# Performance work log

Hardware: AMD Instinct MI355X
Metric: run time of the kernel (lower is better)

The kernel has to match this reference:

```python
import jax, jax.numpy as jnp
import numpy as np

K = 4096          # input_size
N = 12288         # output_size
M = 4096          # tokens (batch*seq)
GROUP_SIZE = 128  # EXL2 quantization group size along K
G = K // GROUP_SIZE


def setup_inputs() -> dict:
    key = jax.random.key(0)
    k1, k2, k3, k4, k5 = jax.random.split(key, 5)
    input_ = jax.random.normal(k1, (M, K), dtype=jnp.float16)
    # packed 4-bit weights: 8 nibbles per int32 along K -> [K//8, N]
    q_weight = jax.random.randint(k2, (K // 8, N), 0, 2147483647, dtype=jnp.int32)
    # packed 4-bit scale codes: 8 per int32 along N -> [G, N//8]
    q_scale = jax.random.randint(k3, (G, N // 8), 0, 2147483647, dtype=jnp.int32)
    # per-group max scale (post_init divides by 256)
    q_scale_max = (jax.random.uniform(k4, (G,), dtype=jnp.float32) / 256.0).astype(jnp.float16)
    q_invperm = jax.random.permutation(k5, jnp.arange(K, dtype=jnp.int32))
    bias = jnp.zeros((N,), dtype=jnp.float16)
    return {"input_": input_, "q_weight": q_weight, "q_scale": q_scale,
            "q_scale_max": q_scale_max, "q_invperm": q_invperm, "bias": bias}


def _dequant(q_weight, q_scale, q_scale_max):
    # unpack 8 4-bit weight codes per int32 along K
    shifts = jnp.arange(8, dtype=jnp.int32) * 4
    wn = (q_weight[:, None, :] >> shifts[None, :, None]) & 0xF   # [K//8, 8, N]
    wn = wn.reshape(K, N).astype(jnp.float32)
    # unpack 8 4-bit scale codes per int32 along N
    sn = (q_scale[:, :, None] >> shifts[None, None, :]) & 0xF    # [G, N//8, 8]
    sn = sn.reshape(G, N).astype(jnp.float32)
    # exllamav2 scale law: s = (code + 1)^2 * scale_max (per group)
    scale = (sn + 1.0) ** 2 * q_scale_max.astype(jnp.float32)[:, None]  # [G, N]
    scale = jnp.repeat(scale, GROUP_SIZE, axis=0)                # [K, N]
    return (wn - 8.0) * scale                                    # dequantized fp32 [K, N]


def reference(input_, q_weight, q_scale, q_scale_max, q_invperm, bias):
    W = _dequant(q_weight, q_scale, q_scale_max)                 # [K, N] fp32
    perm = jnp.argsort(q_invperm)                                # q_perm from post_init
    x = input_.astype(jnp.float32)[:, perm]                      # permuted activations [M, K]
    out = jnp.matmul(x, W).astype(jnp.float16)                   # fused dequant-GEMM result
    return out + bias
```

## Files before the change

### kernel.cpp

```cpp
#include <hip/hip_runtime.h>

#define Mdim 4096
#define Kdim 4096
#define Ndim 12288

typedef __bf16 bf16x8 __attribute__((ext_vector_type(8)));
typedef float f32x4 __attribute__((ext_vector_type(4)));
typedef unsigned short u16x8 __attribute__((ext_vector_type(8)));
typedef int i32x4 __attribute__((ext_vector_type(4)));

__device__ __forceinline__ unsigned short f2bf(float f) {
    unsigned int u = __builtin_bit_cast(unsigned int, f);
    u += 0x7FFFu + ((u >> 16) & 1u);
    return (unsigned short)(u >> 16);
}

typedef __attribute__((address_space(1))) void gvoid_t;
typedef __attribute__((address_space(3))) void lvoid_t;
__device__ __forceinline__ void gld16(const void* g, void* l) {
    __builtin_amdgcn_global_load_lds((gvoid_t*)g, (lvoid_t*)l, 16, 0, 0);
}

__global__ __launch_bounds__(256) void permute_convert_a_kernel(
    const float* __restrict__ A, const int* __restrict__ invperm,
    unsigned short* __restrict__ Ab)
{
    __shared__ unsigned short rowbuf[2][Kdim];
    const int tid = threadIdx.x;
    const int m0 = blockIdx.x * 2;
#pragma unroll
    for (int c = 0; c < 4; ++c) {
        const int i = (c * 256 + tid) * 4;
        const i32x4 ip = *(const i32x4*)&invperm[i];
        const f32x4 v0 = *(const f32x4*)&A[(size_t)m0 * Kdim + i];
        const f32x4 v1 = *(const f32x4*)&A[(size_t)(m0 + 1) * Kdim + i];
#pragma unroll
        for (int u = 0; u < 4; ++u) {
            rowbuf[0][ip[u]] = f2bf(v0[u]);
            rowbuf[1][ip[u]] = f2bf(v1[u]);
        }
    }
    __syncthreads();
#pragma unroll
    for (int r = 0; r < 2; ++r)
#pragma unroll
        for (int c = 0; c < 2; ++c) {
            const int j = (c * 256 + tid) * 8;
            const u16x8 o = *(const u16x8*)&rowbuf[r][j];
            *(u16x8*)&Ab[(size_t)(m0 + r) * Kdim + j] = o;
        }
}

__global__ __launch_bounds__(256) void dequant_kernel(
    const int* __restrict__ qw,
    const int* __restrict__ qs,
    const float* __restrict__ qsm,
    unsigned short* __restrict__ Wt)
{
    __shared__ unsigned short tile[64 * 72];
    const int k0 = blockIdx.x * 64;
    const int n0 = blockIdx.y * 64;
    const int g = k0 >> 7;
    const int tid = threadIdx.x;
    const int n_l = tid & 63;
    const int kb_l = tid >> 6;
    const int n = n0 + n_l;
    const int sw = qs[g * (Ndim / 8) + (n >> 3)];
    const int sc = (sw >> ((n & 7) * 4)) & 0xF;
    const float scale = (float)((sc + 1) * (sc + 1)) * qsm[g];
#pragma unroll
    for (int ii = 0; ii < 2; ++ii) {
        const int kb = kb_l + ii * 4;
        const int w = qw[(size_t)(k0 / 8 + kb) * Ndim + n];
        u16x8 o;
#pragma unroll
        for (int u = 0; u < 8; ++u)
            o[u] = f2bf((float)(((w >> (4 * u)) & 0xF) - 8) * scale);
        *(u16x8*)&tile[n_l * 72 + kb * 8] = o;
    }
    __syncthreads();
#pragma unroll
    for (int cc = 0; cc < 2; ++cc) {
        const int c = tid + cc * 256;
        const int row = c >> 3, part = c & 7;
        const u16x8 v = *(const u16x8*)&tile[row * 72 + part * 8];
        *(u16x8*)&Wt[(size_t)(n0 + row) * Kdim + k0 + part * 8] = v;
    }
}

#define BAR()    asm volatile("s_barrier" ::: "memory")
#define VMCNT8() asm volatile("s_waitcnt vmcnt(8)" ::: "memory")

#define STAGE(dstW, src, slot, koff) do {                                   \
    gld16((src) + (koff), (dstW) + (slot) * 8192);                          \
    gld16((src) + (koff) + rstep, (dstW) + (slot) * 8192 + 4096); } while (0)

#define LD_A(slot, mh) do {                                                 \
    const unsigned short* p_ = &As[slot][wm * 4096 + (mh) * 2048 + aOff];   \
    af[0] = *(const bf16x8*)(p_);                                           \
    af[1] = *(const bf16x8*)(p_ + 512);                                     \
    af[2] = *(const bf16x8*)(p_ + 1024);                                    \
    af[3] = *(const bf16x8*)(p_ + 1536); } while (0)

#define LD_B(slot) do {                                                     \
    const unsigned short* p_ = &Bs[slot][wn * 2048 + aOff];                 \
    bf[0] = *(const bf16x8*)(p_);                                           \
    bf[1] = *(const bf16x8*)(p_ + 512);                                     \
    bf[2] = *(const bf16x8*)(p_ + 1024);                                    \
    bf[3] = *(const bf16x8*)(p_ + 1536); } while (0)

#define MFMA_HALF(mh) do {                                                  \
    __builtin_amdgcn_s_setprio(1);                                          \
    _Pragma("unroll")                                                       \
    for (int i_ = 0; i_ < 4; ++i_)                                          \
      _Pragma("unroll")                                                     \
      for (int j_ = 0; j_ < 4; ++j_)                                        \
        acc[(mh) * 4 + i_][j_] = __builtin_amdgcn_mfma_f32_16x16x32_bf16(   \
            af[i_], bf[j_], acc[(mh) * 4 + i_][j_], 0, 0, 0);               \
    __builtin_amdgcn_s_setprio(0); } while (0)

__global__ __launch_bounds__(512, 2) void gemm_bf16_256_kernel(
    const unsigned short* __restrict__ A,
    const unsigned short* __restrict__ Bt,
    const float* __restrict__ bias,
    float* __restrict__ C)
{
    __shared__ __attribute__((aligned(16))) unsigned short As[4][8192];
    __shared__ __attribute__((aligned(16))) unsigned short Bs[4][8192];

    const int tid = threadIdx.x;
    const int lane = tid & 63, wave = tid >> 6;
    const int wm = wave >> 2, wn = wave & 3;

    const int wgid = (blockIdx.x & 7) * 96 + (blockIdx.x >> 3);
    const int bm = wgid & 15;
    const int bn = wgid >> 4;

    const int srow = 16 * wave + (lane & 15);
    const int skoff = (lane >> 4) * 8;
    const unsigned short* Ag = A + (size_t)(bm * 256 + srow) * Kdim + skoff;
    const unsigned short* Bg = Bt + (size_t)(bn * 256 + srow) * Kdim + skoff;
    const size_t rstep = (size_t)128 * Kdim;
    unsigned short* AsW = &As[0][0] + wave * 512;
    unsigned short* BsW = &Bs[0][0] + wave * 512;

    const int aOff = lane * 8;

    f32x4 acc[8][4];
    const f32x4 zero = {0.f, 0.f, 0.f, 0.f};
#pragma unroll
    for (int i = 0; i < 8; ++i)
#pragma unroll
        for (int j = 0; j < 4; ++j) acc[i][j] = zero;

    STAGE(AsW, Ag, 0, 0);
    STAGE(BsW, Bg, 0, 0);
    STAGE(AsW, Ag, 1, 32);
    STAGE(BsW, Bg, 1, 32);
    STAGE(AsW, Ag, 2, 64);
    STAGE(BsW, Bg, 2, 64);
    VMCNT8();
    BAR();

    bf16x8 af[4], bf[4];
#pragma unroll 2
    for (int t = 0; t < 64; ++t) {
        const int s0 = (2 * t) & 3, s1 = (2 * t + 1) & 3, sd1 = (2 * t + 3) & 3;
        const int tn1 = (t + 1 < 64 ? t + 1 : 63) * 64;
        const int tn2 = (t + 2 < 64 ? t + 2 : 63) * 64;
        LD_A(s0, 0);
        LD_B(s0);
        STAGE(AsW, Ag, sd1, tn1 + 32);
        BAR();
        MFMA_HALF(0);
        BAR();
        LD_A(s0, 1);
        STAGE(BsW, Bg, sd1, tn1 + 32);
        VMCNT8();
        BAR();
        MFMA_HALF(1);
        BAR();
        LD_A(s1, 0);
        LD_B(s1);
        STAGE(AsW, Ag, s0, tn2);
        BAR();
        MFMA_HALF(0);
        BAR();
        LD_A(s1, 1);
        STAGE(BsW, Bg, s0, tn2);
        VMCNT8();
        BAR();
        MFMA_HALF(1);
        BAR();
    }

    const int colb = bn * 256 + wn * 64 + (lane & 15);
    const int rowb = bm * 256 + wm * 128 + (lane >> 4) * 4;
    float bj[4];
#pragma unroll
    for (int j = 0; j < 4; ++j) bj[j] = bias[colb + j * 16];
#pragma unroll
    for (int mf = 0; mf < 8; ++mf)
#pragma unroll
        for (int r = 0; r < 4; ++r) {
            const size_t row = (size_t)(rowb + mf * 16 + r);
#pragma unroll
            for (int j = 0; j < 4; ++j)
                C[row * Ndim + colb + j * 16] = acc[mf][j][r] + bj[j];
        }
}

extern "C" void kernel_launch(void* const* d_in, const int* in_sizes, int n_in,
                              void* d_out, int out_size, void* d_ws, size_t ws_size,
                              hipStream_t stream) {
    const float* input   = (const float*)d_in[0];
    const int*   qw      = (const int*)d_in[1];
    const int*   qs      = (const int*)d_in[2];
    const float* qsm     = (const float*)d_in[3];
    const int*   invperm = (const int*)d_in[4];
    const float* bias    = (const float*)d_in[5];
    float*       out     = (float*)d_out;

    unsigned short* Ab = (unsigned short*)d_ws;
    unsigned short* Wt = (unsigned short*)((char*)d_ws + ((size_t)Mdim * Kdim * 2));

    permute_convert_a_kernel<<<Mdim / 2, 256, 0, stream>>>(input, invperm, Ab);
    dequant_kernel<<<dim3(Kdim / 64, Ndim / 64), 256, 0, stream>>>(qw, qs, qsm, Wt);
    gemm_bf16_256_kernel<<<dim3((Mdim / 256) * (Ndim / 256)), 512, 0, stream>>>(
        Ab, Wt, bias, out);
}
```

Before: 702.6 us.

## Pre-tile A and W into GEMM staging layout for contiguous LDS loads

The permute/convert and dequant kernels now write their bf16 outputs in a blocked layout that matches the GEMM's per-k-step LDS tile order. Each 32-wide k-slice of a 256-row block becomes one contiguous 16 KB chunk, so every thread's global_load_lds reads consecutive addresses instead of strided rows. The permute kernel now handles 16 rows per block to produce whole tiles. This is meant to cut address-translation and strided-fetch overhead in the GEMM main loop, at the cost of more scattered writes in the producer kernels and a larger LDS footprint in the permute kernel.

```diff
diff --git a/kernel.cpp b/kernel.cpp
--- a/kernel.cpp
+++ b/kernel.cpp
@@ -21,34 +21,34 @@
     __builtin_amdgcn_global_load_lds((gvoid_t*)g, (lvoid_t*)l, 16, 0, 0);
 }
 
-__global__ __launch_bounds__(256) void permute_convert_a_kernel(
+
+__global__ __launch_bounds__(512) void permute_convert_a_kernel(
     const float* __restrict__ A, const int* __restrict__ invperm,
     unsigned short* __restrict__ Ab)
 {
-    __shared__ unsigned short rowbuf[2][Kdim];
+    __shared__ unsigned short rowbuf[16][4104];
     const int tid = threadIdx.x;
-    const int m0 = blockIdx.x * 2;
-#pragma unroll
-    for (int c = 0; c < 4; ++c) {
-        const int i = (c * 256 + tid) * 4;
+    const int m0 = blockIdx.x * 16;
+    const int bm = m0 >> 8;
+    const int q  = (m0 >> 4) & 15;
+#pragma unroll
+    for (int c = 0; c < 2; ++c) {
+        const int i = (c * 512 + tid) * 4;
         const i32x4 ip = *(const i32x4*)&invperm[i];
-        const f32x4 v0 = *(const f32x4*)&A[(size_t)m0 * Kdim + i];
-        const f32x4 v1 = *(const f32x4*)&A[(size_t)(m0 + 1) * Kdim + i];
-#pragma unroll
-        for (int u = 0; u < 4; ++u) {
-            rowbuf[0][ip[u]] = f2bf(v0[u]);
-            rowbuf[1][ip[u]] = f2bf(v1[u]);
+        for (int r = 0; r < 16; ++r) {
+            const f32x4 v = *(const f32x4*)&A[(size_t)(m0 + r) * Kdim + i];
+#pragma unroll
+            for (int u = 0; u < 4; ++u) rowbuf[r][ip[u]] = f2bf(v[u]);
         }
     }
     __syncthreads();
-#pragma unroll
-    for (int r = 0; r < 2; ++r)
-#pragma unroll
-        for (int c = 0; c < 2; ++c) {
-            const int j = (c * 256 + tid) * 8;
-            const u16x8 o = *(const u16x8*)&rowbuf[r][j];
-            *(u16x8*)&Ab[(size_t)(m0 + r) * Kdim + j] = o;
-        }
+    unsigned short* dst = Ab + ((size_t)bm << 20) + q * 512;
+    for (int it = 0; it < 16; ++it) {
+        const int c = it * 512 + tid;
+        const int ks = c >> 6, c8 = c & 63;
+        const u16x8 v = *(const u16x8*)&rowbuf[c8 & 15][ks * 32 + (c8 >> 4) * 8];
+        *(u16x8*)&dst[(size_t)ks * 8192 + c8 * 8] = v;
+    }
 }
 
 __global__ __launch_bounds__(256) void dequant_kernel(
@@ -79,21 +79,29 @@
         *(u16x8*)&tile[n_l * 72 + kb * 8] = o;
     }
     __syncthreads();
+    const int bn  = n0 >> 8;
+    const int q0  = (n0 >> 4) & 15;
+    const int ks0 = k0 >> 5;
+    unsigned short* dst = Wt + ((size_t)bn << 20) + (size_t)ks0 * 8192 + q0 * 512;
 #pragma unroll
     for (int cc = 0; cc < 2; ++cc) {
-        const int c = tid + cc * 256;
-        const int row = c >> 3, part = c & 7;
-        const u16x8 v = *(const u16x8*)&tile[row * 72 + part * 8];
-        *(u16x8*)&Wt[(size_t)(n0 + row) * Kdim + k0 + part * 8] = v;
+        const int c  = cc * 256 + tid;
+        const int ksl = c >> 8;
+        const int cq  = (c >> 6) & 3;
+        const int c8  = c & 63;
+        const u16x8 v = *(const u16x8*)
+            &tile[(cq * 16 + (c8 & 15)) * 72 + ksl * 32 + (c8 >> 4) * 8];
+        *(u16x8*)&dst[(size_t)ksl * 8192 + cq * 512 + c8 * 8] = v;
     }
 }
 
 #define BAR()    asm volatile("s_barrier" ::: "memory")
 #define VMCNT8() asm volatile("s_waitcnt vmcnt(8)" ::: "memory")
 
-#define STAGE(dstW, src, slot, koff) do {                                   \
-    gld16((src) + (koff), (dstW) + (slot) * 8192);                          \
-    gld16((src) + (koff) + rstep, (dstW) + (slot) * 8192 + 4096); } while (0)
+#define STAGE(dstW, src, slot, R) do {                                      \
+    gld16((src) + (size_t)(R) * 8192, (dstW) + (slot) * 8192);              \
+    gld16((src) + (size_t)(R) * 8192 + 4096,                                \
+          (dstW) + (slot) * 8192 + 4096); } while (0)
 
 #define LD_A(slot, mh) do {                                                 \
     const unsigned short* p_ = &As[slot][wm * 4096 + (mh) * 2048 + aOff];   \
@@ -136,11 +144,8 @@
     const int bm = wgid & 15;
     const int bn = wgid >> 4;
 
-    const int srow = 16 * wave + (lane & 15);
-    const int skoff = (lane >> 4) * 8;
-    const unsigned short* Ag = A + (size_t)(bm * 256 + srow) * Kdim + skoff;
-    const unsigned short* Bg = Bt + (size_t)(bn * 256 + srow) * Kdim + skoff;
-    const size_t rstep = (size_t)128 * Kdim;
+    const unsigned short* Ag = A + ((size_t)bm << 20) + tid * 8;
+    const unsigned short* Bg = Bt + ((size_t)bn << 20) + tid * 8;
     unsigned short* AsW = &As[0][0] + wave * 512;
     unsigned short* BsW = &Bs[0][0] + wave * 512;
 
@@ -155,10 +160,10 @@
 
     STAGE(AsW, Ag, 0, 0);
     STAGE(BsW, Bg, 0, 0);
-    STAGE(AsW, Ag, 1, 32);
-    STAGE(BsW, Bg, 1, 32);
-    STAGE(AsW, Ag, 2, 64);
-    STAGE(BsW, Bg, 2, 64);
+    STAGE(AsW, Ag, 1, 1);
+    STAGE(BsW, Bg, 1, 1);
+    STAGE(AsW, Ag, 2, 2);
+    STAGE(BsW, Bg, 2, 2);
     VMCNT8();
     BAR();
 
@@ -166,28 +171,28 @@
 #pragma unroll 2
     for (int t = 0; t < 64; ++t) {
         const int s0 = (2 * t) & 3, s1 = (2 * t + 1) & 3, sd1 = (2 * t + 3) & 3;
-        const int tn1 = (t + 1 < 64 ? t + 1 : 63) * 64;
-        const int tn2 = (t + 2 < 64 ? t + 2 : 63) * 64;
+        const int R1 = (2 * t + 3 < 128) ? (2 * t + 3) : 127;
+        const int R2 = (2 * t + 4 < 128) ? (2 * t + 4) : 127;
         LD_A(s0, 0);
         LD_B(s0);
-        STAGE(AsW, Ag, sd1, tn1 + 32);
+        STAGE(AsW, Ag, sd1, R1);
         BAR();
         MFMA_HALF(0);
         BAR();
         LD_A(s0, 1);
-        STAGE(BsW, Bg, sd1, tn1 + 32);
+        STAGE(BsW, Bg, sd1, R1);
         VMCNT8();
         BAR();
         MFMA_HALF(1);
         BAR();
         LD_A(s1, 0);
         LD_B(s1);
-        STAGE(AsW, Ag, s0, tn2);
+        STAGE(AsW, Ag, s0, R2);
         BAR();
         MFMA_HALF(0);
         BAR();
         LD_A(s1, 1);
-        STAGE(BsW, Bg, s0, tn2);
+        STAGE(BsW, Bg, s0, R2);
         VMCNT8();
         BAR();
         MFMA_HALF(1);
@@ -224,7 +229,7 @@
     unsigned short* Ab = (unsigned short*)d_ws;
     unsigned short* Wt = (unsigned short*)((char*)d_ws + ((size_t)Mdim * Kdim * 2));
 
-    permute_convert_a_kernel<<<Mdim / 2, 256, 0, stream>>>(input, invperm, Ab);
+    permute_convert_a_kernel<<<Mdim / 16, 512, 0, stream>>>(input, invperm, Ab);
     dequant_kernel<<<dim3(Kdim / 64, Ndim / 64), 256, 0, stream>>>(qw, qs, qsm, Wt);
     gemm_bf16_256_kernel<<<dim3((Mdim / 256) * (Ndim / 256)), 512, 0, stream>>>(
         Ab, Wt, bias, out);
```

After: 600.3 us. 1.17x faster.
